# Kernel tuning notes

Hardware: AMD Instinct MI355X
Metric: run time of the kernel (lower is better)

The kernel has to match this reference:

```python
import jax, jax.numpy as jnp
import numpy as np
import math

D_MODEL = 1024
NUM_HEADS = 16
D_K = D_MODEL // NUM_HEADS
SEQ_LEN = 2048
THETA = 10000.0


def _rope_tables(seq_len, d_k, theta):
    # inv_freq over even dims, angles repeated-interleaved to full d_k
    inv_freq = theta ** (-jnp.arange(0, d_k, 2, dtype=jnp.float32) / d_k)  # [d_k/2]
    pos = jnp.arange(seq_len, dtype=jnp.float32)                          # [s]
    angles = pos[:, None] * inv_freq[None, :]                             # [s, d_k/2]
    angles = jnp.repeat(angles, 2, axis=-1)                               # [s, d_k]
    return jnp.cos(angles), jnp.sin(angles)


def _rotate_half(x):
    # interleaved pairs: (x0,x1,x2,x3,...) -> (-x1,x0,-x3,x2,...)
    x_even = x[..., ::2]
    x_odd = x[..., 1::2]
    return jnp.stack([-x_odd, x_even], axis=-1).reshape(x.shape)


def _apply_rope(x, cos, sin):
    # x: [b, h, s, d_k]; cos/sin: [s, d_k]
    return x * cos + _rotate_half(x) * sin


def setup_inputs() -> dict:
    key = jax.random.key(0)
    ks = jax.random.split(key, 5)
    scale = 1.0 / math.sqrt(D_MODEL)
    X = jax.random.normal(ks[0], (2, SEQ_LEN, D_MODEL), dtype=jnp.float32)
    Wq = jax.random.normal(ks[1], (D_MODEL, D_MODEL), dtype=jnp.float32) * scale
    Wk = jax.random.normal(ks[2], (D_MODEL, D_MODEL), dtype=jnp.float32) * scale
    Wv = jax.random.normal(ks[3], (D_MODEL, D_MODEL), dtype=jnp.float32) * scale
    Wo = jax.random.normal(ks[4], (D_MODEL, D_MODEL), dtype=jnp.float32) * scale
    return {"X": X, "Wq": Wq, "Wk": Wk, "Wv": Wv, "Wo": Wo}


def reference(X, Wq, Wk, Wv, Wo):
    b, s, _ = X.shape
    h, dk = NUM_HEADS, D_K

    def proj(W):
        return (X @ W.T).reshape(b, s, h, dk).transpose(0, 2, 1, 3)  # [b,h,s,dk]

    q, k, v = proj(Wq), proj(Wk), proj(Wv)

    cos, sin = _rope_tables(s, dk, THETA)
    q = _apply_rope(q, cos, sin)
    k = _apply_rope(k, cos, sin)

    scores = jnp.einsum('bhid,bhjd->bhij', q, k) / math.sqrt(dk)
    causal = jnp.tril(jnp.ones((s, s), dtype=bool))
    scores = jnp.where(causal[None, None], scores, -jnp.inf)
    probs = jax.nn.softmax(scores, axis=-1)
    attended = jnp.einsum('bhij,bhjd->bhid', probs, v)               # [b,h,s,dk]

    out = attended.transpose(0, 2, 1, 3).reshape(b, s, h * dk)
    return out @ Wo.T
```

## Files before the change

### kernel.cpp

```cpp
#include <hip/hip_runtime.h>
#include <stdint.h>

#define D_MODEL 1024
#define NUM_HEADS 16
#define DK 64
#define SEQ 2048
#define BATCH 2
#define MROWS (BATCH * SEQ)
#define LOG2E 1.4426950408889634f
#define FIXM 14.0f

typedef short bf16x8 __attribute__((ext_vector_type(8)));
typedef float f32x4 __attribute__((ext_vector_type(4)));
typedef float f32x16 __attribute__((ext_vector_type(16)));

__device__ __forceinline__ unsigned short f2bf(float f) {
    unsigned int u = __float_as_uint(f);
    u = (u + 0x7fffu + ((u >> 16) & 1u)) >> 16;
    return (unsigned short)u;
}
__device__ __forceinline__ float bf2f(unsigned short h) {
    return __uint_as_float(((unsigned int)h) << 16);
}
__device__ __forceinline__ void async16(const void* g, void* l) {
    __builtin_amdgcn_global_load_lds(
        (const __attribute__((address_space(1))) void*)g,
        (__attribute__((address_space(3))) void*)l, 16, 0, 0);
}
__device__ __forceinline__ unsigned int cvtpk(float lo, float hi) {
    unsigned int r;
    asm("v_cvt_pk_bf16_f32 %0, %1, %2" : "=v"(r) : "v"(lo), "v"(hi));
    return r;
}
#define SWZ64(row, b) ((((row) * 8) + ((b) ^ ((row) & 7))) * 8)

__global__ void cast_all(const float4* __restrict__ X, const float4* __restrict__ Wq,
                         const float4* __restrict__ Wk, const float4* __restrict__ Wv,
                         const float4* __restrict__ Wo, ushort4* __restrict__ Xb,
                         ushort4* __restrict__ Wqkvb, ushort4* __restrict__ Wob) {
    int i = blockIdx.x * blockDim.x + threadIdx.x;
    const float4* src;
    ushort4* dst;
    int off;
    if (i < 1048576) { src = X; dst = Xb; off = i; }
    else if (i < 1310720) { src = Wq; dst = Wqkvb; off = i - 1048576; }
    else if (i < 1572864) { src = Wk; dst = Wqkvb + 262144; off = i - 1310720; }
    else if (i < 1835008) { src = Wv; dst = Wqkvb + 524288; off = i - 1572864; }
    else { src = Wo; dst = Wob; off = i - 1835008; }
    float4 v = src[off];
    ushort4 o;
    o.x = f2bf(v.x); o.y = f2bf(v.y); o.z = f2bf(v.z); o.w = f2bf(v.w);
    dst[off] = o;
}

template <int TN, int OUT_BF16>
__global__ __launch_bounds__(256) void gemm_tile(
    const unsigned short* __restrict__ A, const unsigned short* __restrict__ B,
    void* __restrict__ Cout, int M, int N, int K) {
    __shared__ unsigned short As[128 * 64];
    __shared__ unsigned short Bs[TN * 64];
    const int m0 = blockIdx.y * 128, n0 = blockIdx.x * TN;
    const int t = threadIdx.x;
    const int lane = t & 63, wave = t >> 6;
    const int mA = lane & 15, quad = lane >> 4;
    constexpr int MI = (TN == 128) ? 4 : 2;
    constexpr int NI = 4;
    const int wr = (TN == 128) ? (wave >> 1) * 64 : wave * 32;
    const int wc = (TN == 128) ? (wave & 1) * 64 : 0;

    f32x4 acc[MI][NI] = {};
    for (int k0 = 0; k0 < K; k0 += 64) {
#pragma unroll
        for (int i = 0; i < 4; ++i) {
            int ch = i * 256 + t;
            int r = ch >> 3, b = (ch & 7) ^ (r & 7);
            async16(A + (size_t)(m0 + r) * K + k0 + b * 8, (char*)As + ch * 16);
        }
#pragma unroll
        for (int i = 0; i < TN / 32; ++i) {
            int ch = i * 256 + t;
            int r = ch >> 3, b = (ch & 7) ^ (r & 7);
            async16(B + (size_t)(n0 + r) * K + k0 + b * 8, (char*)Bs + ch * 16);
        }
        __syncthreads();
#pragma unroll
        for (int kk = 0; kk < 2; ++kk) {
            bf16x8 af[MI], bfr[NI];
#pragma unroll
            for (int mi = 0; mi < MI; ++mi) {
                int rr = wr + mi * 16 + mA;
                af[mi] = *(const bf16x8*)&As[SWZ64(rr, kk * 4 + quad)];
            }
#pragma unroll
            for (int ni = 0; ni < NI; ++ni) {
                int rr = wc + ni * 16 + mA;
                bfr[ni] = *(const bf16x8*)&Bs[SWZ64(rr, kk * 4 + quad)];
            }
#pragma unroll
            for (int mi = 0; mi < MI; ++mi)
#pragma unroll
                for (int ni = 0; ni < NI; ++ni)
                    acc[mi][ni] = __builtin_amdgcn_mfma_f32_16x16x32_bf16(
                        af[mi], bfr[ni], acc[mi][ni], 0, 0, 0);
        }
        __syncthreads();
    }
#pragma unroll
    for (int mi = 0; mi < MI; ++mi)
#pragma unroll
        for (int ni = 0; ni < NI; ++ni)
#pragma unroll
            for (int r = 0; r < 4; ++r) {
                int gm = m0 + wr + mi * 16 + quad * 4 + r;
                int gn = n0 + wc + ni * 16 + mA;
                if (OUT_BF16)
                    ((unsigned short*)Cout)[(size_t)gm * N + gn] = f2bf(acc[mi][ni][r]);
                else
                    ((float*)Cout)[(size_t)gm * N + gn] = acc[mi][ni][r];
            }
}

__global__ __launch_bounds__(256) void rope_vt(const unsigned short* __restrict__ QKV,
                                               unsigned short* __restrict__ Qr,
                                               unsigned short* __restrict__ Kr,
                                               unsigned short* __restrict__ Vt) {
    __shared__ unsigned short T[64][80];
    const int bx = blockIdx.x;
    const int t = threadIdx.x;
    if (bx < 4096) {
        int tid = bx * 256 + t;
        int bs = tid >> 8;
        int p4 = tid & 255;
        int b = bs >> 11, spos = bs & 2047;
        int h = p4 >> 4, dd = (p4 & 15) * 4;
        float sn0, cs0, sn1, cs1;
        {
            float if0 = __expf(-(float)dd * (9.210340371976184f / 64.0f));
            float if1 = __expf(-(float)(dd + 2) * (9.210340371976184f / 64.0f));
            __sincosf((float)spos * if0, &sn0, &cs0);
            __sincosf((float)spos * if1, &sn1, &cs1);
        }
        const float SCQ = 0.125f * LOG2E;
        float cs0q = cs0 * SCQ, sn0q = sn0 * SCQ;
        float cs1q = cs1 * SCQ, sn1q = sn1 * SCQ;
        size_t src = (size_t)bs * 3072 + h * 64 + dd;
        ushort4 qw = *(const ushort4*)&QKV[src];
        ushort4 kw = *(const ushort4*)&QKV[src + 1024];
        ushort4 qo_, ko_;
        float e = bf2f(qw.x), o = bf2f(qw.y);
        qo_.x = f2bf(e * cs0q - o * sn0q); qo_.y = f2bf(o * cs0q + e * sn0q);
        e = bf2f(qw.z); o = bf2f(qw.w);
        qo_.z = f2bf(e * cs1q - o * sn1q); qo_.w = f2bf(o * cs1q + e * sn1q);
        e = bf2f(kw.x); o = bf2f(kw.y);
        ko_.x = f2bf(e * cs0 - o * sn0); ko_.y = f2bf(o * cs0 + e * sn0);
        e = bf2f(kw.z); o = bf2f(kw.w);
        ko_.z = f2bf(e * cs1 - o * sn1); ko_.w = f2bf(o * cs1 + e * sn1);
        size_t qb = (((size_t)(b * NUM_HEADS + h) * SEQ + spos) * DK + dd);
        *(ushort4*)&Qr[qb] = qo_;
        *(ushort4*)&Kr[qb] = ko_;
    } else {
        int idx = bx - 4096;
        const int s0 = (idx & 31) * 64, bh = idx >> 5;
        const int b = bh >> 4, h = bh & 15;
#pragma unroll
        for (int i = 0; i < 2; ++i) {
            int ch = i * 256 + t;
            int row = ch >> 3, bc = ch & 7;
            *(int4*)&T[row][bc * 8] =
                *(const int4*)&QKV[(size_t)(b * SEQ + s0 + row) * 3072 + 2048 + h * 64 + bc * 8];
        }
        __syncthreads();
#pragma unroll
        for (int i = 0; i < 2; ++i) {
            int ch = i * 256 + t;
            int d = ch >> 3, sb = ch & 7;
            unsigned short tmp[8];
#pragma unroll
            for (int j = 0; j < 8; ++j) tmp[j] = T[sb * 8 + j][d];
            *(int4*)&Vt[(size_t)bh * DK * SEQ + (size_t)d * SEQ + s0 + sb * 8] = *(int4*)tmp;
        }
    }
}

__global__ __launch_bounds__(256, 4) void flash_attn9(
    const unsigned short* __restrict__ Qr, const unsigned short* __restrict__ Kr,
    const unsigned short* __restrict__ Vt, unsigned short* __restrict__ Att) {
    __shared__ unsigned short Ks[2][64 * 64];
    __shared__ unsigned short Vs[2][64 * 64];
    const int bh = blockIdx.x;
    const int qt = 31 - (int)blockIdx.y;
    const int t = threadIdx.x;
    const int lane = t & 63, wave = t >> 6;
    const int l31 = lane & 31, lh = lane >> 5;
    const int wq = wave >> 1, wd = wave & 1;
    const size_t qkbase = (size_t)bh * SEQ * DK;
    const unsigned short* Kg = Kr + qkbase;
    const unsigned short* Vg = Vt + (size_t)bh * DK * SEQ;
    const int qg = qt * 64 + wq * 32 + l31;

    bf16x8 aq[4];
#pragma unroll
    for (int kk = 0; kk < 4; ++kk)
        aq[kk] = *(const bf16x8*)&Qr[qkbase + (size_t)qg * DK + kk * 16 + lh * 8];

    f32x16 accT;
#pragma unroll
    for (int r = 0; r < 16; ++r) accT[r] = 0.f;
    float la[4] = {0.f, 0.f, 0.f, 0.f};

#pragma unroll
    for (int i = 0; i < 2; ++i) {
        int ch = i * 256 + t;
        int row = ch >> 3, sb = (ch & 7) ^ (row & 7);
        async16(Kg + (size_t)row * DK + sb * 8, (char*)Ks[0] + ch * 16);
        async16(Vg + (size_t)row * SEQ + sb * 8, (char*)Vs[0] + ch * 16);
    }

    for (int jt = 0; jt <= qt; ++jt) {
        __syncthreads();
        const int cur = jt & 1;
        if (jt < qt) {
            const int j1 = (jt + 1) * 64;
#pragma unroll
            for (int i = 0; i < 2; ++i) {
                int ch = i * 256 + t;
                int row = ch >> 3, sb = (ch & 7) ^ (row & 7);
                async16(Kg + (size_t)(j1 + row) * DK + sb * 8, (char*)Ks[cur ^ 1] + ch * 16);
                async16(Vg + (size_t)row * SEQ + j1 + sb * 8, (char*)Vs[cur ^ 1] + ch * 16);
            }
        }
        const unsigned short* Kt = Ks[cur];
        const unsigned short* Vtile = Vs[cur];
        const bool diag = (jt == qt);
        const bool do1 = !(diag && wq == 0);

        f32x16 s0, s1;
#pragma unroll
        for (int r = 0; r < 16; ++r) { s0[r] = 0.f; s1[r] = 0.f; }
        __builtin_amdgcn_s_setprio(1);
#pragma unroll
        for (int kk = 0; kk < 4; ++kk) {
            bf16x8 kf0 = *(const bf16x8*)&Kt[SWZ64(l31, kk * 2 + lh)];
            s0 = __builtin_amdgcn_mfma_f32_32x32x16_bf16(kf0, aq[kk], s0, 0, 0, 0);
            if (do1) {
                bf16x8 kf1 = *(const bf16x8*)&Kt[SWZ64(32 + l31, kk * 2 + lh)];
                s1 = __builtin_amdgcn_mfma_f32_32x32x16_bf16(kf1, aq[kk], s1, 0, 0, 0);
            }
        }
        __builtin_amdgcn_s_setprio(0);
        if (diag) {
            if (wq == 0) {
#pragma unroll
                for (int r = 0; r < 16; ++r) {
                    int crow = (r & 3) + 8 * (r >> 2) + 4 * lh;
                    if (crow > l31) s0[r] = -1e30f;
                }
            } else {
#pragma unroll
                for (int r = 0; r < 16; ++r) {
                    int crow = (r & 3) + 8 * (r >> 2) + 4 * lh;
                    if (crow > l31) s1[r] = -1e30f;
                }
            }
        }

#pragma unroll
        for (int r = 0; r < 16; ++r) {
            s0[r] = __builtin_amdgcn_exp2f(s0[r] - FIXM);
            la[r & 3] += s0[r];
        }
        if (do1) {
#pragma unroll
            for (int r = 0; r < 16; ++r) {
                s1[r] = __builtin_amdgcn_exp2f(s1[r] - FIXM);
                la[r & 3] += s1[r];
            }
        }

        bf16x8 fr[4];
        {
            unsigned int u0 = cvtpk(s0[0], s0[1]), v0 = cvtpk(s0[4], s0[5]);
            unsigned int u1 = cvtpk(s0[2], s0[3]), v1 = cvtpk(s0[6], s0[7]);
            asm("v_permlane32_swap_b32 %0, %1" : "+v"(u0), "+v"(v0));
            asm("v_permlane32_swap_b32 %0, %1" : "+v"(u1), "+v"(v1));
            uint4 w = {u0, u1, v0, v1};
            fr[0] = *(bf16x8*)&w;
            unsigned int u2 = cvtpk(s0[8], s0[9]), v2 = cvtpk(s0[12], s0[13]);
            unsigned int u3 = cvtpk(s0[10], s0[11]), v3 = cvtpk(s0[14], s0[15]);
            asm("v_permlane32_swap_b32 %0, %1" : "+v"(u2), "+v"(v2));
            asm("v_permlane32_swap_b32 %0, %1" : "+v"(u3), "+v"(v3));
            uint4 w2_ = {u2, u3, v2, v3};
            fr[1] = *(bf16x8*)&w2_;
        }
        if (do1) {
            unsigned int u0 = cvtpk(s1[0], s1[1]), v0 = cvtpk(s1[4], s1[5]);
            unsigned int u1 = cvtpk(s1[2], s1[3]), v1 = cvtpk(s1[6], s1[7]);
            asm("v_permlane32_swap_b32 %0, %1" : "+v"(u0), "+v"(v0));
            asm("v_permlane32_swap_b32 %0, %1" : "+v"(u1), "+v"(v1));
            uint4 w = {u0, u1, v0, v1};
            fr[2] = *(bf16x8*)&w;
            unsigned int u2 = cvtpk(s1[8], s1[9]), v2 = cvtpk(s1[12], s1[13]);
            unsigned int u3 = cvtpk(s1[10], s1[11]), v3 = cvtpk(s1[14], s1[15]);
            asm("v_permlane32_swap_b32 %0, %1" : "+v"(u2), "+v"(v2));
            asm("v_permlane32_swap_b32 %0, %1" : "+v"(u3), "+v"(v3));
            uint4 w2_ = {u2, u3, v2, v3};
            fr[3] = *(bf16x8*)&w2_;
        }

        __builtin_amdgcn_s_setprio(1);
#pragma unroll
        for (int kk = 0; kk < 2; ++kk) {
            bf16x8 vf = *(const bf16x8*)&Vtile[SWZ64(wd * 32 + l31, kk * 2 + lh)];
            accT = __builtin_amdgcn_mfma_f32_32x32x16_bf16(vf, fr[kk], accT, 0, 0, 0);
        }
        if (do1) {
#pragma unroll
            for (int kk = 2; kk < 4; ++kk) {
                bf16x8 vf = *(const bf16x8*)&Vtile[SWZ64(wd * 32 + l31, kk * 2 + lh)];
                accT = __builtin_amdgcn_mfma_f32_32x32x16_bf16(vf, fr[kk], accT, 0, 0, 0);
            }
        }
        __builtin_amdgcn_s_setprio(0);
    }

    float lt = (la[0] + la[1]) + (la[2] + la[3]);
    lt += __shfl_xor(lt, 32, 64);
    const float rl = 1.0f / lt;

    const int b_ = bh >> 4, h_ = bh & 15;
#pragma unroll
    for (int rg = 0; rg < 4; ++rg) {
        ushort4 o;
        o.x = f2bf(accT[rg * 4 + 0] * rl);
        o.y = f2bf(accT[rg * 4 + 1] * rl);
        o.z = f2bf(accT[rg * 4 + 2] * rl);
        o.w = f2bf(accT[rg * 4 + 3] * rl);
        *(ushort4*)&Att[(size_t)(b_ * SEQ + qg) * D_MODEL + h_ * DK + wd * 32 + 8 * rg + 4 * lh] = o;
    }
}

extern "C" void kernel_launch(void* const* d_in, const int* in_sizes, int n_in,
                              void* d_out, int out_size, void* d_ws, size_t ws_size,
                              hipStream_t stream) {
    const float* X = (const float*)d_in[0];
    const float* Wq = (const float*)d_in[1];
    const float* Wk = (const float*)d_in[2];
    const float* Wv = (const float*)d_in[3];
    const float* Wo = (const float*)d_in[4];

    char* ws = (char*)d_ws;
    unsigned short* Xb     = (unsigned short*)(ws + 0);
    unsigned short* Wqkvb  = (unsigned short*)(ws + (8u << 20));
    unsigned short* Wob    = (unsigned short*)(ws + (14u << 20));
    unsigned short* QKVraw = (unsigned short*)(ws + (16u << 20));
    unsigned short* Kr     = (unsigned short*)(ws + (40u << 20));
    unsigned short* Vt     = (unsigned short*)(ws + (48u << 20));
    unsigned short* Qr     = Xb;
    unsigned short* Att    = QKVraw;

    cast_all<<<8192, 256, 0, stream>>>((const float4*)X, (const float4*)Wq,
                                       (const float4*)Wk, (const float4*)Wv,
                                       (const float4*)Wo, (ushort4*)Xb,
                                       (ushort4*)Wqkvb, (ushort4*)Wob);

    gemm_tile<128, 1><<<dim3(3072 / 128, MROWS / 128), 256, 0, stream>>>(
        Xb, Wqkvb, QKVraw, MROWS, 3072, D_MODEL);

    rope_vt<<<4096 + 1024, 256, 0, stream>>>(QKVraw, Qr, Kr, Vt);

    flash_attn9<<<dim3(BATCH * NUM_HEADS, 32), 256, 0, stream>>>(Qr, Kr, Vt, Att);

    gemm_tile<64, 0><<<dim3(D_MODEL / 64, MROWS / 128), 256, 0, stream>>>(
        Att, Wob, d_out, MROWS, D_MODEL, D_MODEL);
}
```

Baseline: 186.2 us.

## Split attention key tiles across waves to remove duplicated QK and softmax work

```diff
diff --git a/kernel.cpp b/kernel.cpp
--- a/kernel.cpp
+++ b/kernel.cpp
@@ -182,7 +182,7 @@
     }
 }
 
-__global__ __launch_bounds__(256, 4) void flash_attn9(
+__global__ __launch_bounds__(256, 4) void flash_attn10(
     const unsigned short* __restrict__ Qr, const unsigned short* __restrict__ Kr,
     const unsigned short* __restrict__ Vt, unsigned short* __restrict__ Att) {
     __shared__ unsigned short Ks[2][64 * 64];
@@ -203,9 +203,9 @@
     for (int kk = 0; kk < 4; ++kk)
         aq[kk] = *(const bf16x8*)&Qr[qkbase + (size_t)qg * DK + kk * 16 + lh * 8];
 
-    f32x16 accT;
-#pragma unroll
-    for (int r = 0; r < 16; ++r) accT[r] = 0.f;
+    f32x16 acc0, acc1;
+#pragma unroll
+    for (int r = 0; r < 16; ++r) { acc0[r] = 0.f; acc1[r] = 0.f; }
     float la[4] = {0.f, 0.f, 0.f, 0.f};
 
 #pragma unroll
@@ -232,109 +232,96 @@
         const unsigned short* Kt = Ks[cur];
         const unsigned short* Vtile = Vs[cur];
         const bool diag = (jt == qt);
-        const bool do1 = !(diag && wq == 0);
-
-        f32x16 s0, s1;
-#pragma unroll
-        for (int r = 0; r < 16; ++r) { s0[r] = 0.f; s1[r] = 0.f; }
+        if (diag && wd > wq) continue;
+
+        f32x16 s;
+#pragma unroll
+        for (int r = 0; r < 16; ++r) s[r] = 0.f;
         __builtin_amdgcn_s_setprio(1);
 #pragma unroll
         for (int kk = 0; kk < 4; ++kk) {
-            bf16x8 kf0 = *(const bf16x8*)&Kt[SWZ64(l31, kk * 2 + lh)];
-            s0 = __builtin_amdgcn_mfma_f32_32x32x16_bf16(kf0, aq[kk], s0, 0, 0, 0);
-            if (do1) {
-                bf16x8 kf1 = *(const bf16x8*)&Kt[SWZ64(32 + l31, kk * 2 + lh)];
-                s1 = __builtin_amdgcn_mfma_f32_32x32x16_bf16(kf1, aq[kk], s1, 0, 0, 0);
-            }
+            bf16x8 kf = *(const bf16x8*)&Kt[SWZ64(wd * 32 + l31, kk * 2 + lh)];
+            s = __builtin_amdgcn_mfma_f32_32x32x16_bf16(kf, aq[kk], s, 0, 0, 0);
         }
         __builtin_amdgcn_s_setprio(0);
-        if (diag) {
-            if (wq == 0) {
-#pragma unroll
-                for (int r = 0; r < 16; ++r) {
-                    int crow = (r & 3) + 8 * (r >> 2) + 4 * lh;
-                    if (crow > l31) s0[r] = -1e30f;
-                }
-            } else {
-#pragma unroll
-                for (int r = 0; r < 16; ++r) {
-                    int crow = (r & 3) + 8 * (r >> 2) + 4 * lh;
-                    if (crow > l31) s1[r] = -1e30f;
-                }
+        if (diag && wd == wq) {
+#pragma unroll
+            for (int r = 0; r < 16; ++r) {
+                int crow = (r & 3) + 8 * (r >> 2) + 4 * lh;
+                if (crow > l31) s[r] = -1e30f;
             }
         }
 
 #pragma unroll
         for (int r = 0; r < 16; ++r) {
-            s0[r] = __builtin_amdgcn_exp2f(s0[r] - FIXM);
-            la[r & 3] += s0[r];
-        }
-        if (do1) {
-#pragma unroll
-            for (int r = 0; r < 16; ++r) {
-                s1[r] = __builtin_amdgcn_exp2f(s1[r] - FIXM);
-                la[r & 3] += s1[r];
-            }
-        }
-
-        bf16x8 fr[4];
+            s[r] = __builtin_amdgcn_exp2f(s[r] - FIXM);
+            la[r & 3] += s[r];
+        }
+
+        bf16x8 frA, frB;
         {
-            unsigned int u0 = cvtpk(s0[0], s0[1]), v0 = cvtpk(s0[4], s0[5]);
-            unsigned int u1 = cvtpk(s0[2], s0[3]), v1 = cvtpk(s0[6], s0[7]);
+            unsigned int u0 = cvtpk(s[0], s[1]), v0 = cvtpk(s[4], s[5]);
+            unsigned int u1 = cvtpk(s[2], s[3]), v1 = cvtpk(s[6], s[7]);
             asm("v_permlane32_swap_b32 %0, %1" : "+v"(u0), "+v"(v0));
             asm("v_permlane32_swap_b32 %0, %1" : "+v"(u1), "+v"(v1));
             uint4 w = {u0, u1, v0, v1};
-            fr[0] = *(bf16x8*)&w;
-            unsigned int u2 = cvtpk(s0[8], s0[9]), v2 = cvtpk(s0[12], s0[13]);
-            unsigned int u3 = cvtpk(s0[10], s0[11]), v3 = cvtpk(s0[14], s0[15]);
+            frA = *(bf16x8*)&w;
+            unsigned int u2 = cvtpk(s[8], s[9]), v2 = cvtpk(s[12], s[13]);
+            unsigned int u3 = cvtpk(s[10], s[11]), v3 = cvtpk(s[14], s[15]);
             asm("v_permlane32_swap_b32 %0, %1" : "+v"(u2), "+v"(v2));
             asm("v_permlane32_swap_b32 %0, %1" : "+v"(u3), "+v"(v3));
             uint4 w2_ = {u2, u3, v2, v3};
-            fr[1] = *(bf16x8*)&w2_;
-        }
-        if (do1) {
-            unsigned int u0 = cvtpk(s1[0], s1[1]), v0 = cvtpk(s1[4], s1[5]);
-            unsigned int u1 = cvtpk(s1[2], s1[3]), v1 = cvtpk(s1[6], s1[7]);
-            asm("v_permlane32_swap_b32 %0, %1" : "+v"(u0), "+v"(v0));
-            asm("v_permlane32_swap_b32 %0, %1" : "+v"(u1), "+v"(v1));
-            uint4 w = {u0, u1, v0, v1};
-            fr[2] = *(bf16x8*)&w;
-            unsigned int u2 = cvtpk(s1[8], s1[9]), v2 = cvtpk(s1[12], s1[13]);
-            unsigned int u3 = cvtpk(s1[10], s1[11]), v3 = cvtpk(s1[14], s1[15]);
-            asm("v_permlane32_swap_b32 %0, %1" : "+v"(u2), "+v"(v2));
-            asm("v_permlane32_swap_b32 %0, %1" : "+v"(u3), "+v"(v3));
-            uint4 w2_ = {u2, u3, v2, v3};
-            fr[3] = *(bf16x8*)&w2_;
+            frB = *(bf16x8*)&w2_;
         }
 
         __builtin_amdgcn_s_setprio(1);
-#pragma unroll
-        for (int kk = 0; kk < 2; ++kk) {
-            bf16x8 vf = *(const bf16x8*)&Vtile[SWZ64(wd * 32 + l31, kk * 2 + lh)];
-            accT = __builtin_amdgcn_mfma_f32_32x32x16_bf16(vf, fr[kk], accT, 0, 0, 0);
-        }
-        if (do1) {
-#pragma unroll
-            for (int kk = 2; kk < 4; ++kk) {
-                bf16x8 vf = *(const bf16x8*)&Vtile[SWZ64(wd * 32 + l31, kk * 2 + lh)];
-                accT = __builtin_amdgcn_mfma_f32_32x32x16_bf16(vf, fr[kk], accT, 0, 0, 0);
-            }
+        {
+            bf16x8 vf0 = *(const bf16x8*)&Vtile[SWZ64(l31, (wd * 2 + 0) * 2 + lh)];
+            acc0 = __builtin_amdgcn_mfma_f32_32x32x16_bf16(vf0, frA, acc0, 0, 0, 0);
+            bf16x8 vf1 = *(const bf16x8*)&Vtile[SWZ64(l31, (wd * 2 + 1) * 2 + lh)];
+            acc0 = __builtin_amdgcn_mfma_f32_32x32x16_bf16(vf1, frB, acc0, 0, 0, 0);
+            bf16x8 vf2 = *(const bf16x8*)&Vtile[SWZ64(32 + l31, (wd * 2 + 0) * 2 + lh)];
+            acc1 = __builtin_amdgcn_mfma_f32_32x32x16_bf16(vf2, frA, acc1, 0, 0, 0);
+            bf16x8 vf3 = *(const bf16x8*)&Vtile[SWZ64(32 + l31, (wd * 2 + 1) * 2 + lh)];
+            acc1 = __builtin_amdgcn_mfma_f32_32x32x16_bf16(vf3, frB, acc1, 0, 0, 0);
         }
         __builtin_amdgcn_s_setprio(0);
     }
 
     float lt = (la[0] + la[1]) + (la[2] + la[3]);
     lt += __shfl_xor(lt, 32, 64);
-    const float rl = 1.0f / lt;
+    __syncthreads();
+    float* SC = (float*)Ks;
+    float* LS = (float*)Vs;
+    if (wd == 0) {
+#pragma unroll
+        for (int r = 0; r < 16; ++r) SC[(wq * 2 + 1) * 1024 + r * 64 + lane] = acc1[r];
+    } else {
+#pragma unroll
+        for (int r = 0; r < 16; ++r) SC[(wq * 2 + 0) * 1024 + r * 64 + lane] = acc0[r];
+    }
+    if (lane < 32) LS[wave * 32 + l31] = lt;
+    __syncthreads();
+    const float rl = 1.0f / (LS[(wq * 2) * 32 + l31] + LS[(wq * 2 + 1) * 32 + l31]);
+    float outv[16];
+    if (wd == 0) {
+#pragma unroll
+        for (int r = 0; r < 16; ++r)
+            outv[r] = acc0[r] + SC[(wq * 2 + 0) * 1024 + r * 64 + lane];
+    } else {
+#pragma unroll
+        for (int r = 0; r < 16; ++r)
+            outv[r] = acc1[r] + SC[(wq * 2 + 1) * 1024 + r * 64 + lane];
+    }
 
     const int b_ = bh >> 4, h_ = bh & 15;
 #pragma unroll
     for (int rg = 0; rg < 4; ++rg) {
         ushort4 o;
-        o.x = f2bf(accT[rg * 4 + 0] * rl);
-        o.y = f2bf(accT[rg * 4 + 1] * rl);
-        o.z = f2bf(accT[rg * 4 + 2] * rl);
-        o.w = f2bf(accT[rg * 4 + 3] * rl);
+        o.x = f2bf(outv[rg * 4 + 0] * rl);
+        o.y = f2bf(outv[rg * 4 + 1] * rl);
+        o.z = f2bf(outv[rg * 4 + 2] * rl);
+        o.w = f2bf(outv[rg * 4 + 3] * rl);
         *(ushort4*)&Att[(size_t)(b_ * SEQ + qg) * D_MODEL + h_ * DK + wd * 32 + 8 * rg + 4 * lh] = o;
     }
 }
@@ -368,7 +355,7 @@
 
     rope_vt<<<4096 + 1024, 256, 0, stream>>>(QKVraw, Qr, Kr, Vt);
 
-    flash_attn9<<<dim3(BATCH * NUM_HEADS, 32), 256, 0, stream>>>(Qr, Kr, Vt, Att);
+    flash_attn10<<<dim3(BATCH * NUM_HEADS, 32), 256, 0, stream>>>(Qr, Kr, Vt, Att);
 
     gemm_tile<64, 0><<<dim3(D_MODEL / 64, MROWS / 128), 256, 0, stream>>>(
         Att, Wob, d_out, MROWS, D_MODEL, D_MODEL);
```

New measurement: 175.0 us. 1.06x faster.
